# Performance work log

Hardware: AMD Instinct MI355X
Metric: run time of the kernel (lower is better)

Reference implementation:

```python
import math
import jax, jax.numpy as jnp
import numpy as np

N_BITS = 8
QN = -(2 ** (N_BITS - 1)) + 1   # -127
QP = 2 ** (N_BITS - 1) - 1      # 127
MSB = 1 << (N_BITS - 1)         # 128
SHAPE = (4096, 8192)
FLIP_NUM = 3356  # ceil(numel * 1e-4)


def setup_inputs() -> dict:
    key = jax.random.key(0)
    k1, k2, k3 = jax.random.split(key, 3)
    weight = jax.random.normal(k1, SHAPE, dtype=jnp.float32) * 0.05
    # alpha ~ LSQ init scale magnitude: 2*mean|w|/sqrt(Qp) ~= 0.007; keep positive
    alpha = jax.random.uniform(k2, (1,), dtype=jnp.float32, minval=0.005, maxval=0.02)
    flip_idx = jax.random.randint(k3, (FLIP_NUM,), 0, SHAPE[0] * SHAPE[1], dtype=jnp.int64)
    return {"weight": weight, "alpha": alpha, "flip_idx": flip_idx}


def _grad_scale(x, g):
    # forward: x ; backward: grad * g
    xg = x * g
    return xg + jax.lax.stop_gradient(x - xg)


def _round_pass(x):
    # forward: round(x) ; backward: identity (STE)
    return x + jax.lax.stop_gradient(jnp.round(x) - x)


def reference(weight, alpha, flip_idx):
    numel = weight.size
    g = 1.0 / math.sqrt(numel * QP)
    alpha_c = jnp.maximum(alpha, 1e-4)           # alpha.data.clamp_(min=1e-4)
    a = _grad_scale(alpha_c, g)                  # [1], broadcasts
    q = jnp.clip(weight / a, QN, QP)             # clamp to [Qn, Qp]
    # bit-flip injection: XOR MSB of the truncated-int value at sampled indices,
    # done in-place on .data in torch (no autograd record) -> stop_gradient here
    qf = q.reshape(-1)
    v = qf[flip_idx]
    flipped = jnp.bitwise_xor(v.astype(jnp.int32), MSB).astype(qf.dtype)
    qf = qf.at[flip_idx].set(jax.lax.stop_gradient(flipped))
    q = qf.reshape(weight.shape)
    w_q = _round_pass(q) * a
    return w_q
```

## Files before the change

### kernel.cpp

```cpp
#include <hip/hip_runtime.h>

#define QN_F (-127.0f)
#define QP_F (127.0f)
#define MSB 128

typedef float f32x4 __attribute__((ext_vector_type(4)));

__global__ void quant_main_kernel(const f32x4* __restrict__ w4,
                                  const float* __restrict__ alpha,
                                  f32x4* __restrict__ out4,
                                  int n4) {
    const float a = fmaxf(alpha[0], 1e-4f);
    int idx = blockIdx.x * blockDim.x + threadIdx.x;
    const int stride = gridDim.x * blockDim.x;
    #pragma unroll 4
    for (int i = idx; i < n4; i += stride) {
        f32x4 v = w4[i];
        f32x4 r;
        r.x = rintf(fminf(fmaxf(v.x / a, QN_F), QP_F)) * a;
        r.y = rintf(fminf(fmaxf(v.y / a, QN_F), QP_F)) * a;
        r.z = rintf(fminf(fmaxf(v.z / a, QN_F), QP_F)) * a;
        r.w = rintf(fminf(fmaxf(v.w / a, QN_F), QP_F)) * a;
        __builtin_nontemporal_store(r, &out4[i]);
    }
}

__global__ void flip_fixup_kernel(const float* __restrict__ w,
                                  const float* __restrict__ alpha,
                                  const int* __restrict__ flip_idx,
                                  float* __restrict__ out,
                                  int nf) {
    const float a = fmaxf(alpha[0], 1e-4f);
    int t = blockIdx.x * blockDim.x + threadIdx.x;
    if (t < nf) {
        int i = flip_idx[t];
        float q = fminf(fmaxf(w[i] / a, QN_F), QP_F);
        int qi = (int)q;
        qi ^= MSB;
        out[i] = (float)qi * a;
    }
}

extern "C" void kernel_launch(void* const* d_in, const int* in_sizes, int n_in,
                              void* d_out, int out_size, void* d_ws, size_t ws_size,
                              hipStream_t stream) {
    const float* w = (const float*)d_in[0];
    const float* alpha = (const float*)d_in[1];
    const int* flip_idx = (const int*)d_in[2];
    float* out = (float*)d_out;

    const int n = in_sizes[0];
    const int nf = in_sizes[2];
    const int n4 = n / 4;

    const int block = 256;
    int grid = (n4 + block - 1) / block;
    if (grid > 2048) grid = 2048;
    quant_main_kernel<<<grid, block, 0, stream>>>(
        (const f32x4*)w, alpha, (f32x4*)out, n4);

    int fgrid = (nf + block - 1) / block;
    flip_fixup_kernel<<<fgrid, block, 0, stream>>>(w, alpha, flip_idx, out, nf);
}
```

Measured before the change: 48.31 us.

## Fuse bit-flip fixup into main quantization kernel with contiguous per-block ranges

Merges the two launches into one kernel. Each block now handles a contiguous chunk of the tensor, and after a block barrier it scans the whole flip index list and patches only the indices that fall inside its own chunk. This removes the second launch and the dependency gap between kernels. The cost is that every block reads all ~3.4K flip indices (2048 blocks times 3356 loads, mostly from L2), and the per-block contiguous partition changes the access pattern compared with the grid-stride loop.

```diff
diff --git a/kernel.cpp b/kernel.cpp
--- a/kernel.cpp
+++ b/kernel.cpp
@@ -6,15 +6,22 @@
 
 typedef float f32x4 __attribute__((ext_vector_type(4)));
 
-__global__ void quant_main_kernel(const f32x4* __restrict__ w4,
-                                  const float* __restrict__ alpha,
-                                  f32x4* __restrict__ out4,
-                                  int n4) {
+__global__ void quant_fused_kernel(const float* __restrict__ w,
+                                   const float* __restrict__ alpha,
+                                   const int* __restrict__ flip_idx,
+                                   float* __restrict__ out,
+                                   int n4, int nf) {
     const float a = fmaxf(alpha[0], 1e-4f);
-    int idx = blockIdx.x * blockDim.x + threadIdx.x;
-    const int stride = gridDim.x * blockDim.x;
+
+    const int per_block = (n4 + gridDim.x - 1) / gridDim.x;
+    const int lo4 = blockIdx.x * per_block;
+    const int hi4 = min(lo4 + per_block, n4);
+
+    const f32x4* __restrict__ w4 = (const f32x4*)w;
+    f32x4* __restrict__ out4 = (f32x4*)out;
+
     #pragma unroll 4
-    for (int i = idx; i < n4; i += stride) {
+    for (int i = lo4 + (int)threadIdx.x; i < hi4; i += (int)blockDim.x) {
         f32x4 v = w4[i];
         f32x4 r;
         r.x = rintf(fminf(fmaxf(v.x / a, QN_F), QP_F)) * a;
@@ -23,21 +30,19 @@
         r.w = rintf(fminf(fmaxf(v.w / a, QN_F), QP_F)) * a;
         __builtin_nontemporal_store(r, &out4[i]);
     }
-}
 
-__global__ void flip_fixup_kernel(const float* __restrict__ w,
-                                  const float* __restrict__ alpha,
-                                  const int* __restrict__ flip_idx,
-                                  float* __restrict__ out,
-                                  int nf) {
-    const float a = fmaxf(alpha[0], 1e-4f);
-    int t = blockIdx.x * blockDim.x + threadIdx.x;
-    if (t < nf) {
+    __syncthreads();
+
+    const int loF = lo4 * 4;
+    const int hiF = hi4 * 4;
+    for (int t = (int)threadIdx.x; t < nf; t += (int)blockDim.x) {
         int i = flip_idx[t];
-        float q = fminf(fmaxf(w[i] / a, QN_F), QP_F);
-        int qi = (int)q;
-        qi ^= MSB;
-        out[i] = (float)qi * a;
+        if (i >= loF && i < hiF) {
+            float q = fminf(fmaxf(w[i] / a, QN_F), QP_F);
+            int qi = (int)q;
+            qi ^= MSB;
+            out[i] = (float)qi * a;
+        }
     }
 }
 
@@ -54,11 +59,6 @@
     const int n4 = n / 4;
 
     const int block = 256;
-    int grid = (n4 + block - 1) / block;
-    if (grid > 2048) grid = 2048;
-    quant_main_kernel<<<grid, block, 0, stream>>>(
-        (const f32x4*)w, alpha, (f32x4*)out, n4);
-
-    int fgrid = (nf + block - 1) / block;
-    flip_fixup_kernel<<<fgrid, block, 0, stream>>>(w, alpha, flip_idx, out, nf);
+    const int grid = 2048;
+    quant_fused_kernel<<<grid, block, 0, stream>>>(w, alpha, flip_idx, out, n4, nf);
 }
```

Result: no change. 47.95 us (-0.7%).
